# Performance work log

Hardware: AMD Instinct MI355X
Metric: run time of the kernel (lower is better)

The kernel has to match this reference:

```python
import jax, jax.numpy as jnp
import numpy as np
import math

B, S, D, H = 2, 2048, 1024, 16
DH = D // H
MASK_VALUE = -1e6


def setup_inputs() -> dict:
    key = jax.random.key(0)
    ks = jax.random.split(key, 6)
    x = jax.random.normal(ks[0], (B, S, D), dtype=jnp.float32)
    scale = 1.0 / math.sqrt(D)
    Wq = jax.random.normal(ks[1], (D, D), dtype=jnp.float32) * scale
    Wk = jax.random.normal(ks[2], (D, D), dtype=jnp.float32) * scale
    Wv = jax.random.normal(ks[3], (D, D), dtype=jnp.float32) * scale
    Wo = jax.random.normal(ks[4], (D, D), dtype=jnp.float32) * scale
    valid_lens = jax.random.randint(ks[5], (B,), 1, S + 1, dtype=jnp.int32)
    return {"x": x, "Wq": Wq, "Wk": Wk, "Wv": Wv, "Wo": Wo, "valid_lens": valid_lens}


def reference(x, Wq, Wk, Wv, Wo, valid_lens):
    # Projections (Linear with bias=False): [B,S,D] -> split into H heads of DH
    def split_heads(y):
        return y.reshape(B, S, H, DH).transpose(0, 2, 1, 3)  # [B,H,S,DH]

    q = split_heads(x @ Wq)
    k = split_heads(x @ Wk)
    v = split_heads(x @ Wv)

    # scores [B,H,Sq,Sk]; masking depends only on key position per batch
    scores = jnp.einsum("bhqd,bhkd->bhqk", q, k) / math.sqrt(DH)
    key_pos = jnp.arange(S, dtype=jnp.int32)  # [Sk]
    mask = key_pos[None, None, None, :] < valid_lens[:, None, None, None]
    scores = jnp.where(mask, scores, MASK_VALUE)
    attn = jax.nn.softmax(scores, axis=-1)  # dropout is identity in eval

    out = jnp.einsum("bhqk,bhkd->bhqd", attn, v)  # [B,H,S,DH]
    out = out.transpose(0, 2, 1, 3).reshape(B, S, D)  # concat heads
    return out @ Wo
```

## Files before the change

### kernel.cpp

```cpp
#include <hip/hip_runtime.h>

#define Bdim 2
#define Sdim 2048
#define Ddim 1024
#define Hdim 16

typedef unsigned short u16;
typedef u16 u16x8 __attribute__((ext_vector_type(8)));
typedef u16 u16x4 __attribute__((ext_vector_type(4)));
typedef unsigned u32x4 __attribute__((ext_vector_type(4)));
typedef __bf16 bf16x8 __attribute__((ext_vector_type(8)));
typedef float f32x4 __attribute__((ext_vector_type(4)));
typedef float f32x16 __attribute__((ext_vector_type(16)));

static __device__ __forceinline__ u16 f2bf(float f) {
  unsigned u = __float_as_uint(f);
  u += 0x7fffu + ((u >> 16) & 1u);
  return (u16)(u >> 16);
}
static __device__ __forceinline__ float bf2f(u16 v) {
  return __uint_as_float((unsigned)v << 16);
}
static __device__ __forceinline__ bf16x8 asbf(u16x8 v) {
  return __builtin_bit_cast(bf16x8, v);
}
static __device__ __forceinline__ f32x4 mfma16(bf16x8 a, bf16x8 b, f32x4 c) {
  return __builtin_amdgcn_mfma_f32_16x16x32_bf16(a, b, c, 0, 0, 0);
}
static __device__ __forceinline__ f32x16 mfma32(bf16x8 a, bf16x8 b, f32x16 c) {
  return __builtin_amdgcn_mfma_f32_32x32x16_bf16(a, b, c, 0, 0, 0);
}

static __device__ __forceinline__ size_t tcell(int R, int k) {
  return ((size_t)(R >> 7) * 16 + (k >> 6)) * 1024 + (R & 127) * 8 + ((k >> 3) & 7);
}

__global__ __launch_bounds__(256) void cvtx(const float* __restrict__ x,
                                            u16* __restrict__ xt) {
  int i = blockIdx.x * 256 + threadIdx.x;
  const float4* xp = (const float4*)x;
  float4 a = xp[2 * i], b = xp[2 * i + 1];
  u16x8 o;
  o[0] = f2bf(a.x); o[1] = f2bf(a.y); o[2] = f2bf(a.z); o[3] = f2bf(a.w);
  o[4] = f2bf(b.x); o[5] = f2bf(b.y); o[6] = f2bf(b.z); o[7] = f2bf(b.w);
  int R = i >> 7, k = (i & 127) * 8;
  ((u16x8*)xt)[tcell(R, k)] = o;
}

__global__ __launch_bounds__(256) void transw(
    const float* __restrict__ W0, const float* __restrict__ W1,
    const float* __restrict__ W2, const float* __restrict__ W3,
    u16* __restrict__ T0, u16* __restrict__ T1,
    u16* __restrict__ T2, u16* __restrict__ T3) {
  const float* W = blockIdx.z == 0 ? W0 : blockIdx.z == 1 ? W1 : blockIdx.z == 2 ? W2 : W3;
  u16* T = blockIdx.z == 0 ? T0 : blockIdx.z == 1 ? T1 : blockIdx.z == 2 ? T2 : T3;
  __shared__ float tile[32][33];
  const int t = threadIdx.x;
  const int k0 = blockIdx.x * 32, n0 = blockIdx.y * 32;
  const int r = t >> 3, cq = (t & 7) * 4;
  float4 v = *(const float4*)(W + (size_t)(k0 + r) * Ddim + n0 + cq);
  tile[r][cq] = v.x; tile[r][cq + 1] = v.y; tile[r][cq + 2] = v.z; tile[r][cq + 3] = v.w;
  __syncthreads();
  u16x4 ov;
  ov[0] = f2bf(tile[cq][r]);
  ov[1] = f2bf(tile[cq + 1][r]);
  ov[2] = f2bf(tile[cq + 2][r]);
  ov[3] = f2bf(tile[cq + 3][r]);
  int n = n0 + r, k = k0 + cq;
  *(u16x4*)(T + tcell(n, k) * 8 + (k & 7)) = ov;
}

__global__ __launch_bounds__(256) void gemm_qkv(
    const u16* __restrict__ A,
    const u16* __restrict__ Bt0, const u16* __restrict__ Bt1, const u16* __restrict__ Bt2,
    u16* __restrict__ Qt, u16* __restrict__ Kt, u16* __restrict__ Vt) {
  __shared__ u16 As[128 * 64];
  __shared__ u16 Bs[128 * 64];
  const int zz = blockIdx.y >> 3;
  const u16* Bt = (zz == 0) ? Bt0 : (zz == 1) ? Bt1 : Bt2;

  const int t = threadIdx.x;
  const int lane = t & 63, w = t >> 6;
  const int wm = w >> 1, wn = w & 1;
  const int c = lane & 15, g = lane >> 4;
  const int mb = blockIdx.x, nb = blockIdx.y & 7;
  const float oscale = (zz == 0) ? 0.125f : 1.0f;

  const f32x4 zv = {0.f, 0.f, 0.f, 0.f};
  f32x4 acc[4][4];
#pragma unroll
  for (int m = 0; m < 4; m++)
#pragma unroll
    for (int n = 0; n < 4; n++) acc[m][n] = zv;

  const u16x8* Ac = (const u16x8*)A;
  const u16x8* Bc = (const u16x8*)Bt;
  u16x8 ra[4], rb[4];
#pragma unroll
  for (int i = 0; i < 4; i++) {
    ra[i] = Ac[(size_t)(mb * 16 + 0) * 1024 + t + 256 * i];
    rb[i] = Bc[(size_t)(nb * 16 + 0) * 1024 + t + 256 * i];
  }
#pragma unroll
  for (int i = 0; i < 4; i++) {
    int idx = t + 256 * i;
    int row = idx >> 3, ch = idx & 7;
    int sw = (ch ^ (row & 7)) * 8;
    *(u16x8*)(As + row * 64 + sw) = ra[i];
    *(u16x8*)(Bs + row * 64 + sw) = rb[i];
  }
  __syncthreads();

  for (int kt = 0; kt < 16; ++kt) {
    const bool more = (kt + 1) < 16;
    if (more) {
#pragma unroll
      for (int i = 0; i < 4; i++) {
        ra[i] = Ac[(size_t)(mb * 16 + kt + 1) * 1024 + t + 256 * i];
        rb[i] = Bc[(size_t)(nb * 16 + kt + 1) * 1024 + t + 256 * i];
      }
    }
#pragma unroll
    for (int kh = 0; kh < 2; kh++) {
      bf16x8 af[4], bfr[4];
#pragma unroll
      for (int m = 0; m < 4; m++) {
        int row = wm * 64 + m * 16 + c;
        int chr = kh * 4 + g;
        af[m] = asbf(*(const u16x8*)(As + row * 64 + ((chr ^ (row & 7)) * 8)));
      }
#pragma unroll
      for (int n = 0; n < 4; n++) {
        int row = wn * 64 + n * 16 + c;
        int chr = kh * 4 + g;
        bfr[n] = asbf(*(const u16x8*)(Bs + row * 64 + ((chr ^ (row & 7)) * 8)));
      }
#pragma unroll
      for (int m = 0; m < 4; m++)
#pragma unroll
        for (int n = 0; n < 4; n++) acc[m][n] = mfma16(af[m], bfr[n], acc[m][n]);
    }
    if (more) {
      __syncthreads();
#pragma unroll
      for (int i = 0; i < 4; i++) {
        int idx = t + 256 * i;
        int row = idx >> 3, ch = idx & 7;
        int sw = (ch ^ (row & 7)) * 8;
        *(u16x8*)(As + row * 64 + sw) = ra[i];
        *(u16x8*)(Bs + row * 64 + sw) = rb[i];
      }
      __syncthreads();
    }
  }
  if (zz < 2) {
    u16* Ct = (zz == 0) ? Qt : Kt;
#pragma unroll
    for (int m = 0; m < 4; m++)
#pragma unroll
      for (int n = 0; n < 4; n++) {
        int col = nb * 128 + wn * 64 + n * 16 + c;
        int Rb = mb * 128 + wm * 64 + m * 16 + 4 * g;
        size_t base = ((size_t)((Rb >> 11) * 16 + (col >> 6)) * 32 + ((Rb >> 6) & 31)) * 4096 +
                      ((col & 63) >> 3) * 512 + (size_t)(Rb & 63) * 8 + (col & 7);
#pragma unroll
        for (int r = 0; r < 4; r++)
          Ct[base + (size_t)r * 8] = f2bf(acc[m][n][r] * oscale);
      }
  } else {
#pragma unroll
    for (int m = 0; m < 4; m++)
#pragma unroll
      for (int n = 0; n < 4; n++) {
        int col = nb * 128 + wn * 64 + n * 16 + c;
        int Rb = mb * 128 + wm * 64 + m * 16 + 4 * g;
        u16x4 ov;
#pragma unroll
        for (int r = 0; r < 4; r++) ov[r] = f2bf(acc[m][n][r]);
        size_t addr = ((size_t)((Rb >> 11) * 16 + (col >> 6)) * 32 + ((Rb >> 6) & 31)) * 4096 +
                      ((Rb & 63) >> 3) * 512 + (size_t)(col & 63) * 8 + (Rb & 7);
        *(u16x4*)(Vt + addr) = ov;
      }
  }
}

__global__ __launch_bounds__(256) void gemm_wo(
    const u16* __restrict__ A, const u16* __restrict__ Bt, float* __restrict__ C) {
  __shared__ u16 As[64 * 64];
  __shared__ u16 Bs[64 * 64];
  const int t = threadIdx.x;
  const int lane = t & 63, w = t >> 6;
  const int wm = w >> 1, wn = w & 1;
  const int c = lane & 15, g = lane >> 4;
  const int mb = blockIdx.x, nb = blockIdx.y;

  const f32x4 zv = {0.f, 0.f, 0.f, 0.f};
  f32x4 acc[2][2];
#pragma unroll
  for (int m = 0; m < 2; m++)
#pragma unroll
    for (int n = 0; n < 2; n++) acc[m][n] = zv;

  const u16x8* Ac = (const u16x8*)A;
  const u16x8* Bc = (const u16x8*)Bt;
  const size_t abase = (size_t)(mb >> 1) * 16384 + (size_t)(mb & 1) * 512;
  const size_t bbase = (size_t)(nb >> 1) * 16384 + (size_t)(nb & 1) * 512;
  u16x8 ra[2], rb[2];
#pragma unroll
  for (int i = 0; i < 2; i++) {
    ra[i] = Ac[abase + 0 * 1024 + t + 256 * i];
    rb[i] = Bc[bbase + 0 * 1024 + t + 256 * i];
  }
  {
#pragma unroll
    for (int i = 0; i < 2; i++) {
      int idx = t + 256 * i;
      int row = idx >> 3, ch = idx & 7;
      int sw = (ch ^ (row & 7)) * 8;
      *(u16x8*)(As + row * 64 + sw) = ra[i];
      *(u16x8*)(Bs + row * 64 + sw) = rb[i];
    }
  }
  __syncthreads();

  for (int kt = 0; kt < 16; ++kt) {
    const bool more = (kt + 1) < 16;
    if (more) {
#pragma unroll
      for (int i = 0; i < 2; i++) {
        ra[i] = Ac[abase + (size_t)(kt + 1) * 1024 + t + 256 * i];
        rb[i] = Bc[bbase + (size_t)(kt + 1) * 1024 + t + 256 * i];
      }
    }
#pragma unroll
    for (int kh = 0; kh < 2; kh++) {
      bf16x8 af[2], bfr[2];
#pragma unroll
      for (int m = 0; m < 2; m++) {
        int row = wm * 32 + m * 16 + c;
        int chr = kh * 4 + g;
        af[m] = asbf(*(const u16x8*)(As + row * 64 + ((chr ^ (row & 7)) * 8)));
      }
#pragma unroll
      for (int n = 0; n < 2; n++) {
        int row = wn * 32 + n * 16 + c;
        int chr = kh * 4 + g;
        bfr[n] = asbf(*(const u16x8*)(Bs + row * 64 + ((chr ^ (row & 7)) * 8)));
      }
#pragma unroll
      for (int m = 0; m < 2; m++)
#pragma unroll
        for (int n = 0; n < 2; n++) acc[m][n] = mfma16(af[m], bfr[n], acc[m][n]);
    }
    if (more) {
      __syncthreads();
#pragma unroll
      for (int i = 0; i < 2; i++) {
        int idx = t + 256 * i;
        int row = idx >> 3, ch = idx & 7;
        int sw = (ch ^ (row & 7)) * 8;
        *(u16x8*)(As + row * 64 + sw) = ra[i];
        *(u16x8*)(Bs + row * 64 + sw) = rb[i];
      }
      __syncthreads();
    }
  }
#pragma unroll
  for (int m = 0; m < 2; m++)
#pragma unroll
    for (int n = 0; n < 2; n++)
#pragma unroll
      for (int r = 0; r < 4; r++) {
        int row = mb * 64 + wm * 32 + m * 16 + 4 * g + r;
        int col = nb * 64 + wn * 32 + n * 16 + c;
        C[(size_t)row * 1024 + col] = acc[m][n][r];
      }
}

__global__ __launch_bounds__(64, 4) void attn_kernel(
    const u16* __restrict__ Qt, const u16* __restrict__ Kt,
    const u16* __restrict__ Vt, const int* __restrict__ vlen,
    u16* __restrict__ O, u16* __restrict__ Opart, float2* __restrict__ mlp) {
  __shared__ u16 ot[32][72];
  const int lane = threadIdx.x;
  const int q = lane & 31, hi = lane >> 5;
  const int bh = blockIdx.y, b = bh >> 4, h = bh & 15;
  const int q0 = blockIdx.x * 32;
  const int nv = vlen[b];
  const int NS = gridDim.z, z = blockIdx.z;

  bf16x8 qf[4];
  {
    const u16* Qtile = Qt + ((size_t)bh * 32 + (q0 >> 6)) * 4096;
    int qrow = (q0 & 63) + q;
#pragma unroll
    for (int s = 0; s < 4; s++)
      qf[s] = asbf(*(const u16x8*)(Qtile + (2 * s + hi) * 512 + qrow * 8));
  }

  f32x16 o0, o1;
#pragma unroll
  for (int r = 0; r < 16; r++) { o0[r] = 0.f; o1[r] = 0.f; }
  float m = -3.0e38f, l = 0.f;

  const int nt = (nv + 63) >> 6;
  const int chunk = (nt + NS - 1) / NS;
  const int t0 = z * chunk;
  const int t1 = min(nt, t0 + chunk);
  for (int kt = t0; kt < t1; ++kt) {
    const int k0 = kt * 64;
    const u16* Ktile = Kt + ((size_t)bh * 32 + kt) * 4096;
    const u16* Vtile = Vt + ((size_t)bh * 32 + kt) * 4096;
    f32x16 sc[2];
#pragma unroll
    for (int kb = 0; kb < 2; kb++) {
      f32x16 acc;
#pragma unroll
      for (int r = 0; r < 16; r++) acc[r] = 0.f;
#pragma unroll
      for (int s = 0; s < 4; s++) {
        bf16x8 kf = asbf(*(const u16x8*)(Ktile + (2 * s + hi) * 512 + (kb * 32 + q) * 8));
        acc = mfma32(kf, qf[s], acc);
      }
      sc[kb] = acc;
    }
    if (k0 + 64 > nv) {
#pragma unroll
      for (int kb = 0; kb < 2; kb++)
#pragma unroll
        for (int r = 0; r < 16; r++) {
          int key = k0 + kb * 32 + (r & 3) + 8 * (r >> 2) + 4 * hi;
          if (key >= nv) sc[kb][r] = -1e30f;
        }
    }
    float mx[16];
#pragma unroll
    for (int r = 0; r < 16; r++) mx[r] = fmaxf(sc[0][r], sc[1][r]);
#pragma unroll
    for (int st = 8; st > 0; st >>= 1)
#pragma unroll
      for (int r = 0; r < st; r++) mx[r] = fmaxf(mx[r], mx[r + st]);
    float tm = fmaxf(mx[0], __shfl_xor(mx[0], 32));
    if (!__all(tm <= m + 8.f)) {
      float mn = fmaxf(m, tm);
      float al = __expf(m - mn);
#pragma unroll
      for (int r = 0; r < 16; r++) { o0[r] *= al; o1[r] *= al; }
      l *= al;
      m = mn;
    }
    unsigned pw[4][4];
    float s0 = 0.f, s1 = 0.f, s2 = 0.f, s3 = 0.f;
#pragma unroll
    for (int kb = 0; kb < 2; kb++)
#pragma unroll
      for (int hh = 0; hh < 2; hh++)
#pragma unroll
        for (int wi = 0; wi < 4; wi++) {
          float e0 = __expf(sc[kb][hh * 8 + wi * 2] - m);
          float e1 = __expf(sc[kb][hh * 8 + wi * 2 + 1] - m);
          if (wi == 0) s0 += e0 + e1;
          else if (wi == 1) s1 += e0 + e1;
          else if (wi == 2) s2 += e0 + e1;
          else s3 += e0 + e1;
          asm("v_cvt_pk_bf16_f32 %0, %1, %2"
              : "=v"(pw[kb * 2 + hh][wi]) : "v"(e0), "v"(e1));
        }
    float ssum = (s0 + s1) + (s2 + s3);
    ssum += __shfl_xor(ssum, 32);
    l += ssum;
#pragma unroll
    for (int f = 0; f < 4; f++) {
      asm("v_permlane32_swap_b32 %0, %1" : "+v"(pw[f][0]), "+v"(pw[f][2]));
      asm("v_permlane32_swap_b32 %0, %1" : "+v"(pw[f][1]), "+v"(pw[f][3]));
    }
#pragma unroll
    for (int f = 0; f < 4; f++) {
      u32x4 wv = {pw[f][0], pw[f][1], pw[f][2], pw[f][3]};
      bf16x8 pa = __builtin_bit_cast(bf16x8, wv);
      bf16x8 va = asbf(*(const u16x8*)(Vtile + (2 * f + hi) * 512 + q * 8));
      bf16x8 vb = asbf(*(const u16x8*)(Vtile + (2 * f + hi) * 512 + (32 + q) * 8));
      o0 = mfma32(va, pa, o0);
      o1 = mfma32(vb, pa, o1);
    }
  }
  const float scale = (NS == 1) ? (1.f / l) : 1.f;
#pragma unroll
  for (int r = 0; r < 16; r++) {
    const int dh = (r & 3) + 8 * (r >> 2) + 4 * hi;
    ot[q][dh] = f2bf(o0[r] * scale);
    ot[q][32 + dh] = f2bf(o1[r] * scale);
  }
  asm volatile("s_waitcnt lgkmcnt(0)" ::: "memory");
  __builtin_amdgcn_sched_barrier(0);
  if (NS == 1) {
    int R = b * Sdim + q0 + q;
    size_t cellbase = ((size_t)(R >> 7) * 16 + h) * 1024 + (R & 127) * 8 + hi * 4;
#pragma unroll
    for (int j = 0; j < 4; j++)
      ((u16x8*)O)[cellbase + j] = *(const u16x8*)(&ot[q][hi * 32 + j * 8]);
  } else {
    u16* op = Opart + ((size_t)(z * 32 + bh) * Sdim + q0 + q) * 64 + hi * 32;
#pragma unroll
    for (int j = 0; j < 4; j++)
      *(u16x8*)(op + j * 8) = *(const u16x8*)(&ot[q][hi * 32 + j * 8]);
    if (hi == 0)
      mlp[(size_t)(z * 32 + bh) * Sdim + q0 + q] = make_float2(m, l);
  }
}

template <int NS>
__global__ __launch_bounds__(256) void attn_combine(
    const u16* __restrict__ Opart, const float2* __restrict__ mlp,
    u16* __restrict__ O) {
  const int t = threadIdx.x;
  const int bh = blockIdx.y, b = bh >> 4, h = bh & 15;
  const int q = blockIdx.x * 32 + (t >> 3);
  const int d0 = (t & 7) * 8;
  float2 ml[NS];
  float M = -3.0e38f;
#pragma unroll
  for (int z = 0; z < NS; z++) {
    ml[z] = mlp[(size_t)(z * 32 + bh) * Sdim + q];
    M = fmaxf(M, ml[z].x);
  }
  float acc[8];
#pragma unroll
  for (int i = 0; i < 8; i++) acc[i] = 0.f;
  float wsum = 0.f;
#pragma unroll
  for (int z = 0; z < NS; z++) {
    float w = __expf(ml[z].x - M);
    wsum += w * ml[z].y;
    u16x8 ov = *(const u16x8*)(Opart + ((size_t)(z * 32 + bh) * Sdim + q) * 64 + d0);
#pragma unroll
    for (int i = 0; i < 8; i++) acc[i] += w * bf2f(ov[i]);
  }
  const float inv = 1.f / wsum;
  u16x8 res;
#pragma unroll
  for (int i = 0; i < 8; i++) res[i] = f2bf(acc[i] * inv);
  int R = b * Sdim + q;
  ((u16x8*)O)[((size_t)(R >> 7) * 16 + h) * 1024 + (R & 127) * 8 + (d0 >> 3)] = res;
}

extern "C" void kernel_launch(void* const* d_in, const int* in_sizes, int n_in,
                              void* d_out, int out_size, void* d_ws, size_t ws_size,
                              hipStream_t stream) {
  const float* x = (const float*)d_in[0];
  const float* Wq = (const float*)d_in[1];
  const float* Wk = (const float*)d_in[2];
  const float* Wv = (const float*)d_in[3];
  const float* Wo = (const float*)d_in[4];
  const int* vl = (const int*)d_in[5];
  float* out = (float*)d_out;

  char* ws = (char*)d_ws;
  const size_t SZ_X = (size_t)Bdim * Sdim * Ddim * sizeof(u16);
  const size_t SZ_W = (size_t)Ddim * Ddim * sizeof(u16);
  u16* xt = (u16*)ws; ws += SZ_X;
  u16* WqT = (u16*)ws; ws += SZ_W;
  u16* WkT = (u16*)ws; ws += SZ_W;
  u16* WvT = (u16*)ws; ws += SZ_W;
  u16* WoT = (u16*)ws; ws += SZ_W;
  u16* Qtb = (u16*)ws; ws += SZ_X;
  u16* Ktb = (u16*)ws; ws += SZ_X;
  u16* Vtb = (u16*)ws; ws += SZ_X;
  u16* Obt = (u16*)ws; ws += SZ_X;

  const size_t PER_SPLIT = (size_t)Bdim * Hdim * Sdim * 64 * sizeof(u16) +
                           (size_t)Bdim * Hdim * Sdim * sizeof(float2);
  size_t used = (size_t)(ws - (char*)d_ws);
  size_t avail = (ws_size > used) ? ws_size - used : 0;
  int NS = (avail >= 4 * PER_SPLIT) ? 4 : (avail >= 2 * PER_SPLIT) ? 2 : 1;
  u16* Opart = (u16*)ws;
  float2* mlp = (float2*)(ws + (size_t)NS * Bdim * Hdim * Sdim * 64 * sizeof(u16));

  cvtx<<<dim3((Bdim * Sdim * Ddim) / (8 * 256)), 256, 0, stream>>>(x, xt);
  transw<<<dim3(32, 32, 4), 256, 0, stream>>>(Wq, Wk, Wv, Wo, WqT, WkT, WvT, WoT);
  gemm_qkv<<<dim3(32, 24), 256, 0, stream>>>(xt, WqT, WkT, WvT, Qtb, Ktb, Vtb);
  attn_kernel<<<dim3(Sdim / 32, Bdim * Hdim, NS), 64, 0, stream>>>(Qtb, Ktb, Vtb, vl, Obt,
                                                                   Opart, mlp);
  if (NS == 4)
    attn_combine<4><<<dim3(Sdim / 32, Bdim * Hdim), 256, 0, stream>>>(Opart, mlp, Obt);
  else if (NS == 2)
    attn_combine<2><<<dim3(Sdim / 32, Bdim * Hdim), 256, 0, stream>>>(Opart, mlp, Obt);
  gemm_wo<<<dim3(64, 16), 256, 0, stream>>>(Obt, WoT, out);
}
```

Baseline: 109.2 us.

## Fuse split-KV attention combine into the output projection GEMM A-tile load

Removes the separate attn_combine kernel and instead merges the split-KV partial outputs (using per-row max/sum) while loading A tiles inside the Wo GEMM. This saves a kernel launch and the write and re-read of the combined attention output. In exchange, every column block of the GEMM re-reads all NS partial tiles and recomputes the softmax rescaling, which multiplies partial-output traffic and ALU work in the GEMM prologue.

New measurement: 134.8 us. +23.4%, slower.

```diff
diff --git a/kernel.cpp b/kernel.cpp
--- a/kernel.cpp
+++ b/kernel.cpp
@@ -184,7 +184,132 @@
   }
 }
 
-__global__ __launch_bounds__(256) void gemm_wo(
+template <int NS>
+__global__ __launch_bounds__(256) void gemm_wo_merge(
+    const u16* __restrict__ Opart, const float2* __restrict__ mlp,
+    const u16* __restrict__ Bt, float* __restrict__ C) {
+  __shared__ u16 As[64 * 64];
+  __shared__ u16 Bs[64 * 64];
+  const int t = threadIdx.x;
+  const int lane = t & 63, w = t >> 6;
+  const int wm = w >> 1, wn = w & 1;
+  const int c = lane & 15, g = lane >> 4;
+  const int mb = blockIdx.x, nb = blockIdx.y;
+  const int r0 = t >> 3, ch = t & 7;
+  const int bb = mb >> 5;
+  const int qb = (mb & 31) * 64;
+
+  const f32x4 zv = {0.f, 0.f, 0.f, 0.f};
+  f32x4 acc[2][2];
+#pragma unroll
+  for (int m = 0; m < 2; m++)
+#pragma unroll
+    for (int n = 0; n < 2; n++) acc[m][n] = zv;
+
+  const u16x8* Bc = (const u16x8*)Bt;
+  const size_t bbase = (size_t)(nb >> 1) * 16384 + (size_t)(nb & 1) * 512;
+
+  u16x8 rap[2][NS];
+  float2 ml[2][NS];
+  u16x8 rb[2];
+
+#define LOADA_WO(ktv)                                                          \
+  _Pragma("unroll") for (int i = 0; i < 2; i++) {                              \
+    int q = qb + r0 + 32 * i;                                                  \
+    _Pragma("unroll") for (int z = 0; z < NS; z++) {                           \
+      size_t base = (size_t)(z * 32 + bb * 16 + (ktv)) * 2048 + q;             \
+      rap[i][z] = *(const u16x8*)(Opart + base * 64 + ch * 8);                 \
+      ml[i][z] = mlp[base];                                                    \
+    }                                                                          \
+  }
+#define MERGEA_WO()                                                            \
+  _Pragma("unroll") for (int i = 0; i < 2; i++) {                              \
+    float M = -3.0e38f;                                                        \
+    _Pragma("unroll") for (int z = 0; z < NS; z++) M = fmaxf(M, ml[i][z].x);   \
+    float wt[NS], wsum = 0.f;                                                  \
+    _Pragma("unroll") for (int z = 0; z < NS; z++) {                           \
+      wt[z] = __expf(ml[i][z].x - M);                                          \
+      wsum += wt[z] * ml[i][z].y;                                              \
+    }                                                                          \
+    float inv = 1.f / wsum;                                                    \
+    u16x8 res;                                                                 \
+    _Pragma("unroll") for (int e = 0; e < 8; e++) {                            \
+      float a = 0.f;                                                           \
+      _Pragma("unroll") for (int z = 0; z < NS; z++)                           \
+        a += wt[z] * bf2f(rap[i][z][e]);                                       \
+      res[e] = f2bf(a * inv);                                                  \
+    }                                                                          \
+    int row = r0 + 32 * i;                                                     \
+    *(u16x8*)(As + row * 64 + ((ch ^ (row & 7)) * 8)) = res;                   \
+  }
+
+  LOADA_WO(0);
+#pragma unroll
+  for (int i = 0; i < 2; i++) rb[i] = Bc[bbase + 0 * 1024 + t + 256 * i];
+  MERGEA_WO();
+#pragma unroll
+  for (int i = 0; i < 2; i++) {
+    int idx = t + 256 * i;
+    int row = idx >> 3, chb = idx & 7;
+    *(u16x8*)(Bs + row * 64 + ((chb ^ (row & 7)) * 8)) = rb[i];
+  }
+  __syncthreads();
+
+  for (int kt = 0; kt < 16; ++kt) {
+    const bool more = (kt + 1) < 16;
+    if (more) {
+      LOADA_WO(kt + 1);
+#pragma unroll
+      for (int i = 0; i < 2; i++)
+        rb[i] = Bc[bbase + (size_t)(kt + 1) * 1024 + t + 256 * i];
+    }
+#pragma unroll
+    for (int kh = 0; kh < 2; kh++) {
+      bf16x8 af[2], bfr[2];
+#pragma unroll
+      for (int m = 0; m < 2; m++) {
+        int row = wm * 32 + m * 16 + c;
+        int chr = kh * 4 + g;
+        af[m] = asbf(*(const u16x8*)(As + row * 64 + ((chr ^ (row & 7)) * 8)));
+      }
+#pragma unroll
+      for (int n = 0; n < 2; n++) {
+        int row = wn * 32 + n * 16 + c;
+        int chr = kh * 4 + g;
+        bfr[n] = asbf(*(const u16x8*)(Bs + row * 64 + ((chr ^ (row & 7)) * 8)));
+      }
+#pragma unroll
+      for (int m = 0; m < 2; m++)
+#pragma unroll
+        for (int n = 0; n < 2; n++) acc[m][n] = mfma16(af[m], bfr[n], acc[m][n]);
+    }
+    if (more) {
+      __syncthreads();
+      MERGEA_WO();
+#pragma unroll
+      for (int i = 0; i < 2; i++) {
+        int idx = t + 256 * i;
+        int row = idx >> 3, chb = idx & 7;
+        *(u16x8*)(Bs + row * 64 + ((chb ^ (row & 7)) * 8)) = rb[i];
+      }
+      __syncthreads();
+    }
+  }
+#pragma unroll
+  for (int m = 0; m < 2; m++)
+#pragma unroll
+    for (int n = 0; n < 2; n++)
+#pragma unroll
+      for (int r = 0; r < 4; r++) {
+        int row = mb * 64 + wm * 32 + m * 16 + 4 * g + r;
+        int col = nb * 64 + wn * 32 + n * 16 + c;
+        C[(size_t)row * 1024 + col] = acc[m][n][r];
+      }
+#undef LOADA_WO
+#undef MERGEA_WO
+}
+
+__global__ __launch_bounds__(256) void gemm_wo_plain(
     const u16* __restrict__ A, const u16* __restrict__ Bt, float* __restrict__ C) {
   __shared__ u16 As[64 * 64];
   __shared__ u16 Bs[64 * 64];
@@ -211,15 +336,13 @@
     ra[i] = Ac[abase + 0 * 1024 + t + 256 * i];
     rb[i] = Bc[bbase + 0 * 1024 + t + 256 * i];
   }
-  {
-#pragma unroll
-    for (int i = 0; i < 2; i++) {
-      int idx = t + 256 * i;
-      int row = idx >> 3, ch = idx & 7;
-      int sw = (ch ^ (row & 7)) * 8;
-      *(u16x8*)(As + row * 64 + sw) = ra[i];
-      *(u16x8*)(Bs + row * 64 + sw) = rb[i];
-    }
+#pragma unroll
+  for (int i = 0; i < 2; i++) {
+    int idx = t + 256 * i;
+    int row = idx >> 3, ch = idx & 7;
+    int sw = (ch ^ (row & 7)) * 8;
+    *(u16x8*)(As + row * 64 + sw) = ra[i];
+    *(u16x8*)(Bs + row * 64 + sw) = rb[i];
   }
   __syncthreads();
 
@@ -409,41 +532,6 @@
   }
 }
 
-template <int NS>
-__global__ __launch_bounds__(256) void attn_combine(
-    const u16* __restrict__ Opart, const float2* __restrict__ mlp,
-    u16* __restrict__ O) {
-  const int t = threadIdx.x;
-  const int bh = blockIdx.y, b = bh >> 4, h = bh & 15;
-  const int q = blockIdx.x * 32 + (t >> 3);
-  const int d0 = (t & 7) * 8;
-  float2 ml[NS];
-  float M = -3.0e38f;
-#pragma unroll
-  for (int z = 0; z < NS; z++) {
-    ml[z] = mlp[(size_t)(z * 32 + bh) * Sdim + q];
-    M = fmaxf(M, ml[z].x);
-  }
-  float acc[8];
-#pragma unroll
-  for (int i = 0; i < 8; i++) acc[i] = 0.f;
-  float wsum = 0.f;
-#pragma unroll
-  for (int z = 0; z < NS; z++) {
-    float w = __expf(ml[z].x - M);
-    wsum += w * ml[z].y;
-    u16x8 ov = *(const u16x8*)(Opart + ((size_t)(z * 32 + bh) * Sdim + q) * 64 + d0);
-#pragma unroll
-    for (int i = 0; i < 8; i++) acc[i] += w * bf2f(ov[i]);
-  }
-  const float inv = 1.f / wsum;
-  u16x8 res;
-#pragma unroll
-  for (int i = 0; i < 8; i++) res[i] = f2bf(acc[i] * inv);
-  int R = b * Sdim + q;
-  ((u16x8*)O)[((size_t)(R >> 7) * 16 + h) * 1024 + (R & 127) * 8 + (d0 >> 3)] = res;
-}
-
 extern "C" void kernel_launch(void* const* d_in, const int* in_sizes, int n_in,
                               void* d_out, int out_size, void* d_ws, size_t ws_size,
                               hipStream_t stream) {
@@ -482,8 +570,9 @@
   attn_kernel<<<dim3(Sdim / 32, Bdim * Hdim, NS), 64, 0, stream>>>(Qtb, Ktb, Vtb, vl, Obt,
                                                                    Opart, mlp);
   if (NS == 4)
-    attn_combine<4><<<dim3(Sdim / 32, Bdim * Hdim), 256, 0, stream>>>(Opart, mlp, Obt);
+    gemm_wo_merge<4><<<dim3(64, 16), 256, 0, stream>>>(Opart, mlp, WoT, out);
   else if (NS == 2)
-    attn_combine<2><<<dim3(Sdim / 32, Bdim * Hdim), 256, 0, stream>>>(Opart, mlp, Obt);
-  gemm_wo<<<dim3(64, 16), 256, 0, stream>>>(Obt, WoT, out);
-}
+    gemm_wo_merge<2><<<dim3(64, 16), 256, 0, stream>>>(Opart, mlp, WoT, out);
+  else
+    gemm_wo_plain<<<dim3(64, 16), 256, 0, stream>>>(Obt, WoT, out);
+}
```
